# Kernel tuning notes

Hardware: AMD Instinct MI355X
Metric: run time of the kernel (lower is better)

The kernel has to match this reference:

```python
import jax, jax.numpy as jnp
import numpy as np

B, S, D_IN, D_H = 8, 4096, 256, 512
EPS = 1e-6


def setup_inputs() -> dict:
    key = jax.random.key(0)
    ks = jax.random.split(key, 5)
    scale = 1.0 / np.sqrt(D_IN)  # torch Linear default init scale (uniform bound)
    x = jax.random.normal(ks[0], (B, S, D_IN), dtype=jnp.float32)
    Wi = jax.random.normal(ks[1], (D_IN, D_H), dtype=jnp.float32) * scale
    Wf = jax.random.normal(ks[2], (D_IN, D_H), dtype=jnp.float32) * scale
    Wo = jax.random.normal(ks[3], (D_IN, D_H), dtype=jnp.float32) * scale
    Wz = jax.random.normal(ks[4], (D_IN, D_H), dtype=jnp.float32) * scale
    zb = jnp.zeros((D_H,), dtype=jnp.float32)
    return {"x": x, "Wi": Wi, "bi": zb, "Wf": Wf, "bf": zb,
            "Wo": Wo, "bo": zb, "Wz": Wz, "bz": zb}


def _xlstm_forward(x, Wi, bi, Wf, bf, Wo, bo, Wz, bz):
    # Batched projections over all timesteps at once: [B,S,D_H] each.
    i_t = jnp.exp(jnp.clip(jnp.einsum('bsd,dh->bsh', x, Wi) + bi, -20.0, 0.0))
    f_t = jnp.exp(jnp.clip(jnp.einsum('bsd,dh->bsh', x, Wf) + bf, -20.0, 0.0))
    o_t = jax.nn.sigmoid(jnp.einsum('bsd,dh->bsh', x, Wo) + bo)
    z_t = jnp.tanh(jnp.einsum('bsd,dh->bsh', x, Wz) + bz)

    def step(carry, gates):
        c, n = carry
        i, f, o, z = gates
        c = f * c + i * z
        n = f * n + i
        h = o * (c / (n + EPS))
        return (c, n), h

    c0 = jnp.zeros((x.shape[0], Wi.shape[1]), dtype=x.dtype)
    n0 = jnp.ones((x.shape[0], Wi.shape[1]), dtype=x.dtype)
    # time-major scan over the recurrence
    gates_tm = tuple(jnp.swapaxes(g, 0, 1) for g in (i_t, f_t, o_t, z_t))  # [S,B,H]
    _, h_tm = jax.lax.scan(step, (c0, n0), gates_tm)
    return jnp.swapaxes(h_tm, 0, 1)  # [B,S,H]


def reference(x, Wi, bi, Wf, bf, Wo, bo, Wz, bz):
    return _xlstm_forward(x, Wi, bi, Wf, bf, Wo, bo, Wz, bz)
```

## Files before the change

kernel.cpp:

```cpp
#include <hip/hip_runtime.h>
#include <hip/hip_bf16.h>
#include <cstdint>
#include <cstddef>

typedef __hip_bfloat16 bf16;
typedef __attribute__((ext_vector_type(8))) short short8;
typedef __attribute__((ext_vector_type(4))) short short4v;
typedef __attribute__((ext_vector_type(4))) float floatx4;

#define BB 8
#define SS 4096
#define DIN 256
#define DH 512
#define NCH 256
#define CHUNK 16

__device__ __forceinline__ float b2f(bf16 v) { return __bfloat162float(v); }
__device__ __forceinline__ float sh2f(short v) {
    unsigned int u = ((unsigned int)(unsigned short)v) << 16;
    float f; __builtin_memcpy(&f, &u, 4); return f;
}
__device__ __forceinline__ float frcp(float x) { return __builtin_amdgcn_rcpf(x); }

__global__ __launch_bounds__(256) void convert_x(
    const float* __restrict__ X, bf16* __restrict__ Xb)
{
    const int idx = blockIdx.x * 256 + threadIdx.x;
    float4 v = ((const float4*)X)[idx];
    bf16 o[4] = {__float2bfloat16(v.x), __float2bfloat16(v.y),
                 __float2bfloat16(v.z), __float2bfloat16(v.w)};
    ((short4v*)Xb)[idx] = *(const short4v*)o;
}

__global__ __launch_bounds__(256) void transpose_w(
    const float* __restrict__ Wi, const float* __restrict__ Wf,
    const float* __restrict__ Wo, const float* __restrict__ Wz,
    bf16* __restrict__ Wt)
{
    int o  = blockIdx.x * 256 + threadIdx.x;
    int nf = o >> 8;
    int k  = o & 255;
    int g  = nf >> 9;
    int hh = nf & 511;
    const float* W = (g == 0) ? Wi : (g == 1) ? Wf : (g == 2) ? Wo : Wz;
    Wt[o] = __float2bfloat16(W[(size_t)k * DH + hh]);
}

__device__ __forceinline__ void load16_lds(const bf16* g, short* l)
{
    __builtin_amdgcn_global_load_lds(
        (const __attribute__((address_space(1))) unsigned int*)g,
        (__attribute__((address_space(3))) unsigned int*)l,
        16, 0, 0);
}

__global__ __launch_bounds__(256) void gemm_fused(
    const bf16* __restrict__ Xb, const bf16* __restrict__ Wt,
    const float* __restrict__ bi, const float* __restrict__ bfv,
    const float* __restrict__ bo, const float* __restrict__ bz,
    bf16* __restrict__ Pi, bf16* __restrict__ Pf,
    bf16* __restrict__ Po, bf16* __restrict__ Pz,
    float* __restrict__ Aa, float* __restrict__ Bca, float* __restrict__ Bna,
    int nb)
{
    __shared__ __align__(16) short As[64 * 32];
    __shared__ __align__(16) short Bs[256 * 32];
    __shared__ __align__(16) bf16  Gb[4 * 64 * 64];

    const int tid  = threadIdx.x;
    const int m0   = blockIdx.x * 64;
    const int h0   = blockIdx.y * 64;
    const int wave = tid >> 6, lane = tid & 63;
    const int l15  = lane & 15;
    const int q    = lane >> 4;

    floatx4 acc[4][4];
#pragma unroll
    for (int i = 0; i < 4; i++)
#pragma unroll
        for (int j = 0; j < 4; j++) acc[i][j] = (floatx4){0.f, 0.f, 0.f, 0.f};

    const int rr = tid >> 2;
    const int cc = (tid & 3) * 8;
    const bf16* agp = Xb + (size_t)(m0 + rr) * DIN + cc;
    const bf16* bgp0 = Wt + (size_t)(0 * 512 + h0 + rr) * DIN + cc;
    const bf16* bgp1 = Wt + (size_t)(1 * 512 + h0 + rr) * DIN + cc;
    const bf16* bgp2 = Wt + (size_t)(2 * 512 + h0 + rr) * DIN + cc;
    const bf16* bgp3 = Wt + (size_t)(3 * 512 + h0 + rr) * DIN + cc;

    for (int k0 = 0; k0 < DIN; k0 += 32) {
        load16_lds(agp + k0, &As[tid * 8]);
        load16_lds(bgp0 + k0, &Bs[0 * 2048 + tid * 8]);
        load16_lds(bgp1 + k0, &Bs[1 * 2048 + tid * 8]);
        load16_lds(bgp2 + k0, &Bs[2 * 2048 + tid * 8]);
        load16_lds(bgp3 + k0, &Bs[3 * 2048 + tid * 8]);
        __syncthreads();

        short8 af[4], bfr[4];
#pragma unroll
        for (int ti = 0; ti < 4; ti++)
            af[ti] = *(const short8*)&As[(ti * 16 + l15) * 32 + q * 8];
#pragma unroll
        for (int tj = 0; tj < 4; tj++)
            bfr[tj] = *(const short8*)&Bs[wave * 2048 + (tj * 16 + l15) * 32 + q * 8];
#pragma unroll
        for (int ti = 0; ti < 4; ti++)
#pragma unroll
            for (int tj = 0; tj < 4; tj++)
                acc[ti][tj] = __builtin_amdgcn_mfma_f32_16x16x32_bf16(
                    af[ti], bfr[tj], acc[ti][tj], 0, 0, 0);
        __syncthreads();
    }

    const float* bias = (wave == 0) ? bi : (wave == 1) ? bfv
                      : (wave == 2) ? bo : bz;
    bf16* gb = &Gb[wave * 4096];
#pragma unroll
    for (int ti = 0; ti < 4; ti++) {
#pragma unroll
        for (int tj = 0; tj < 4; tj++) {
            const int h = tj * 16 + l15;
            const float bsv = bias[h0 + h];
#pragma unroll
            for (int r = 0; r < 4; r++) {
                const int s = ti * 16 + q * 4 + r;
                const float v = acc[ti][tj][r] + bsv;
                float a;
                if (wave == 0 || wave == 1)
                    a = __expf(fminf(fmaxf(v, -20.f), 0.f));
                else if (wave == 2)
                    a = frcp(1.f + __expf(-v));
                else
                    a = 1.f - 2.f * frcp(__expf(2.f * v) + 1.f);
                gb[s * 64 + h] = __float2bfloat16(a);
            }
        }
    }
    __syncthreads();

    bf16* const planes[4] = {Pi, Pf, Po, Pz};
#pragma unroll
    for (int p = 0; p < 8; p++) {
        const int cid = p * 256 + tid;
        const int g   = cid >> 9;
        const int rem = cid & 511;
        const int s   = rem >> 3;
        const int c   = rem & 7;
        short8 v8 = *(const short8*)&Gb[g * 4096 + s * 64 + c * 8];
        *(short8*)&planes[g][(size_t)(m0 + s) * DH + h0 + c * 8] = v8;
    }

    {
        const int hh  = tid & 63;
        const int sub = tid >> 6;
        float A = 1.f, Bc = 0.f, Bn = 0.f;
#pragma unroll
        for (int s = 0; s < CHUNK; s++) {
            const int sl = sub * CHUNK + s;
            const float f  = b2f(Gb[1 * 4096 + sl * 64 + hh]);
            const float iv = b2f(Gb[0 * 4096 + sl * 64 + hh]);
            const float zv = b2f(Gb[3 * 4096 + sl * 64 + hh]);
            Bc = fmaf(f, Bc, iv * zv);
            Bn = fmaf(f, Bn, iv);
            A *= f;
        }
        const int b  = m0 >> 12;
        const int s0 = m0 & (SS - 1);
        const int ch = (s0 >> 4) + sub;
        const size_t cidx = ((size_t)ch * nb + b) * DH + h0 + hh;
        Aa[cidx] = A; Bca[cidx] = Bc; Bna[cidx] = Bn;
    }
}

__global__ __launch_bounds__(256) void scan_chunks(
    const float* __restrict__ Aa, const float* __restrict__ Bca,
    const float* __restrict__ Bna,
    float* __restrict__ Cs, float* __restrict__ Ns, int nb)
{
    const int t = blockIdx.x * 256 + threadIdx.x;
    float c = 0.f, n = 1.f;
    for (int ch = 0; ch < NCH; ch++) {
        const size_t cidx = (size_t)ch * (nb * DH) + t;
        Cs[cidx] = c; Ns[cidx] = n;
        const float A = Aa[cidx];
        c = fmaf(A, c, Bca[cidx]);
        n = fmaf(A, n, Bna[cidx]);
    }
}

__global__ __launch_bounds__(256) void scan_emit(
    const bf16* __restrict__ Pi, const bf16* __restrict__ Pf,
    const bf16* __restrict__ Po, const bf16* __restrict__ Pz,
    const float* __restrict__ Cs, const float* __restrict__ Ns,
    float* __restrict__ out, int nb)
{
    const int tid = threadIdx.x;
    const int ch  = blockIdx.x * 4 + (tid >> 6);
    const int b   = blockIdx.y;
    const int hg  = (tid & 63) * 8;
    const size_t base = ((size_t)(b * SS + ch * CHUNK)) * DH + hg;
    const size_t cidx = (size_t)(ch * nb + b) * DH + hg;

    float c[8], n[8];
#pragma unroll
    for (int j = 0; j < 2; j++) {
        *(floatx4*)&c[j * 4] = *(const floatx4*)(Cs + cidx + j * 4);
        *(floatx4*)&n[j * 4] = *(const floatx4*)(Ns + cidx + j * 4);
    }

#pragma unroll 4
    for (int s = 0; s < CHUNK; s++) {
        const size_t o = base + (size_t)s * DH;
        short8 i8 = *(const short8*)(Pi + o);
        short8 f8 = *(const short8*)(Pf + o);
        short8 o8 = *(const short8*)(Po + o);
        short8 z8 = *(const short8*)(Pz + o);
        float h[8];
#pragma unroll
        for (int j = 0; j < 8; j++) {
            const float f  = sh2f(f8[j]);
            const float iv = sh2f(i8[j]);
            const float ov = sh2f(o8[j]);
            const float zv = sh2f(z8[j]);
            c[j] = fmaf(f, c[j], iv * zv);
            n[j] = fmaf(f, n[j], iv);
            h[j] = ov * c[j] * frcp(n[j] + 1e-6f);
        }
        *(floatx4*)(out + o)     = *(floatx4*)&h[0];
        *(floatx4*)(out + o + 4) = *(floatx4*)&h[4];
    }
}

extern "C" void kernel_launch(void* const* d_in, const int* in_sizes, int n_in,
                              void* d_out, int out_size, void* d_ws, size_t ws_size,
                              hipStream_t stream)
{
    const float* x   = (const float*)d_in[0];
    const float* Wi  = (const float*)d_in[1];
    const float* bi  = (const float*)d_in[2];
    const float* Wf  = (const float*)d_in[3];
    const float* bfv = (const float*)d_in[4];
    const float* Wo  = (const float*)d_in[5];
    const float* bo  = (const float*)d_in[6];
    const float* Wz  = (const float*)d_in[7];
    const float* bz  = (const float*)d_in[8];
    float* out = (float*)d_out;

    int nb = BB;
    while (nb > 1) {
        size_t need = (1u << 20)
                    + (size_t)nb * SS * DIN * 2
                    + 4 * (size_t)nb * SS * DH * 2
                    + 5 * (size_t)NCH * nb * DH * 4;
        if (need <= ws_size) break;
        nb >>= 1;
    }

    const size_t plane = (size_t)nb * SS * DH;
    bf16* Wt = (bf16*)d_ws;
    bf16* Xb = (bf16*)((char*)d_ws + (1u << 20));
    bf16* Pi = Xb + (size_t)nb * SS * DIN;
    bf16* Pf = Pi + plane;
    bf16* Po = Pf + plane;
    bf16* Pz = Po + plane;
    float* Aa  = (float*)(Pz + plane);
    float* Bca = Aa  + (size_t)NCH * nb * DH;
    float* Bna = Bca + (size_t)NCH * nb * DH;
    float* Cs  = Bna + (size_t)NCH * nb * DH;
    float* Ns  = Cs  + (size_t)NCH * nb * DH;

    transpose_w<<<2048, 256, 0, stream>>>(Wi, Wf, Wo, Wz, Wt);

    for (int b0 = 0; b0 < BB; b0 += nb) {
        const float* Xsrc = x   + (size_t)b0 * SS * DIN;
        float*       Ob   = out + (size_t)b0 * SS * DH;
        convert_x<<<nb * 1024, 256, 0, stream>>>(Xsrc, Xb);
        gemm_fused<<<dim3(nb * SS / 64, DH / 64), 256, 0, stream>>>(
            Xb, Wt, bi, bfv, bo, bz, Pi, Pf, Po, Pz, Aa, Bca, Bna, nb);
        scan_chunks<<<2 * nb, 256, 0, stream>>>(Aa, Bca, Bna, Cs, Ns, nb);
        scan_emit<<<dim3(NCH / 4, nb), 256, 0, stream>>>(
            Pi, Pf, Po, Pz, Cs, Ns, Ob, nb);
    }
}
```

Before: 253.3 us.

## Recompute gate GEMM in emit pass instead of storing bf16 gate planes

The gate projections are no longer written to four bf16 planes in global memory. A first GEMM pass computes only the i, f and z gates to build per-chunk carries, and a second pass recomputes all four gates and emits the output directly using the scanned chunk states. The weight transpose now uses a shared-memory tiled transpose and is merged with the x conversion into a single prep launch. This trades about 1.75x the GEMM FLOPs for removing roughly 32 MB of plane writes and 32 MB of plane reads.

```diff
diff --git a/kernel.cpp b/kernel.cpp
--- a/kernel.cpp
+++ b/kernel.cpp
@@ -16,34 +16,49 @@
 #define CHUNK 16
 
 __device__ __forceinline__ float b2f(bf16 v) { return __bfloat162float(v); }
-__device__ __forceinline__ float sh2f(short v) {
-    unsigned int u = ((unsigned int)(unsigned short)v) << 16;
-    float f; __builtin_memcpy(&f, &u, 4); return f;
-}
 __device__ __forceinline__ float frcp(float x) { return __builtin_amdgcn_rcpf(x); }
 
-__global__ __launch_bounds__(256) void convert_x(
-    const float* __restrict__ X, bf16* __restrict__ Xb)
-{
-    const int idx = blockIdx.x * 256 + threadIdx.x;
-    float4 v = ((const float4*)X)[idx];
-    bf16 o[4] = {__float2bfloat16(v.x), __float2bfloat16(v.y),
-                 __float2bfloat16(v.z), __float2bfloat16(v.w)};
-    ((short4v*)Xb)[idx] = *(const short4v*)o;
-}
-
-__global__ __launch_bounds__(256) void transpose_w(
+__global__ __launch_bounds__(256) void prep(
+    const float* __restrict__ X, bf16* __restrict__ Xb,
     const float* __restrict__ Wi, const float* __restrict__ Wf,
     const float* __restrict__ Wo, const float* __restrict__ Wz,
-    bf16* __restrict__ Wt)
-{
-    int o  = blockIdx.x * 256 + threadIdx.x;
-    int nf = o >> 8;
-    int k  = o & 255;
-    int g  = nf >> 9;
-    int hh = nf & 511;
+    bf16* __restrict__ Wt, int nconv)
+{
+    __shared__ float tile[32][33];
+    const int tid = threadIdx.x;
+    if ((int)blockIdx.x < nconv) {
+        const int idx = blockIdx.x * 256 + tid;
+        float4 v = ((const float4*)X)[idx];
+        bf16 o[4] = {__float2bfloat16(v.x), __float2bfloat16(v.y),
+                     __float2bfloat16(v.z), __float2bfloat16(v.w)};
+        ((short4v*)Xb)[idx] = *(const short4v*)o;
+        return;
+    }
+    const int beta = blockIdx.x - nconv;
+    const int g   = beta >> 7;
+    const int rem = beta & 127;
+    const int k0  = (rem >> 4) * 32;
+    const int h0  = (rem & 15) * 32;
     const float* W = (g == 0) ? Wi : (g == 1) ? Wf : (g == 2) ? Wo : Wz;
-    Wt[o] = __float2bfloat16(W[(size_t)k * DH + hh]);
+
+    {
+        const int r = tid >> 5;
+        const int c = tid & 31;
+#pragma unroll
+        for (int j = 0; j < 4; j++)
+            tile[r + j * 8][c] = W[(size_t)(k0 + r + j * 8) * DH + h0 + c];
+    }
+    __syncthreads();
+    {
+        const int kw = tid & 31;
+        const int hw = tid >> 5;
+#pragma unroll
+        for (int j = 0; j < 4; j++) {
+            const int h = hw + j * 8;
+            Wt[(size_t)(g * 512 + h0 + h) * DIN + k0 + kw] =
+                __float2bfloat16(tile[kw][h]);
+        }
+    }
 }
 
 __device__ __forceinline__ void load16_lds(const bf16* g, short* l)
@@ -54,18 +69,16 @@
         16, 0, 0);
 }
 
-__global__ __launch_bounds__(256) void gemm_fused(
+__global__ __launch_bounds__(256) void gemm_carry(
     const bf16* __restrict__ Xb, const bf16* __restrict__ Wt,
     const float* __restrict__ bi, const float* __restrict__ bfv,
-    const float* __restrict__ bo, const float* __restrict__ bz,
-    bf16* __restrict__ Pi, bf16* __restrict__ Pf,
-    bf16* __restrict__ Po, bf16* __restrict__ Pz,
+    const float* __restrict__ bz,
     float* __restrict__ Aa, float* __restrict__ Bca, float* __restrict__ Bna,
     int nb)
 {
     __shared__ __align__(16) short As[64 * 32];
-    __shared__ __align__(16) short Bs[256 * 32];
-    __shared__ __align__(16) bf16  Gb[4 * 64 * 64];
+    __shared__ __align__(16) short Bs[3 * 64 * 32];
+    __shared__ __align__(16) bf16  Gb[3 * 64 * 64];
 
     const int tid  = threadIdx.x;
     const int m0   = blockIdx.x * 64;
@@ -73,6 +86,7 @@
     const int wave = tid >> 6, lane = tid & 63;
     const int l15  = lane & 15;
     const int q    = lane >> 4;
+    const int gslice = (wave == 3) ? 2 : wave;
 
     floatx4 acc[4][4];
 #pragma unroll
@@ -82,14 +96,133 @@
 
     const int rr = tid >> 2;
     const int cc = (tid & 3) * 8;
-    const bf16* agp = Xb + (size_t)(m0 + rr) * DIN + cc;
+    const bf16* agp  = Xb + (size_t)(m0 + rr) * DIN + cc;
+    const bf16* bgpi = Wt + (size_t)(0 * 512 + h0 + rr) * DIN + cc;
+    const bf16* bgpf = Wt + (size_t)(1 * 512 + h0 + rr) * DIN + cc;
+    const bf16* bgpz = Wt + (size_t)(3 * 512 + h0 + rr) * DIN + cc;
+
+    for (int k0 = 0; k0 < DIN; k0 += 32) {
+        load16_lds(agp  + k0, &As[tid * 8]);
+        load16_lds(bgpi + k0, &Bs[0 * 2048 + tid * 8]);
+        load16_lds(bgpf + k0, &Bs[1 * 2048 + tid * 8]);
+        load16_lds(bgpz + k0, &Bs[2 * 2048 + tid * 8]);
+        __syncthreads();
+
+        if (wave != 2) {
+            short8 af[4], bfr[4];
+#pragma unroll
+            for (int ti = 0; ti < 4; ti++)
+                af[ti] = *(const short8*)&As[(ti * 16 + l15) * 32 + q * 8];
+#pragma unroll
+            for (int tj = 0; tj < 4; tj++)
+                bfr[tj] = *(const short8*)&Bs[gslice * 2048 + (tj * 16 + l15) * 32 + q * 8];
+#pragma unroll
+            for (int ti = 0; ti < 4; ti++)
+#pragma unroll
+                for (int tj = 0; tj < 4; tj++)
+                    acc[ti][tj] = __builtin_amdgcn_mfma_f32_16x16x32_bf16(
+                        af[ti], bfr[tj], acc[ti][tj], 0, 0, 0);
+        }
+        __syncthreads();
+    }
+
+    if (wave != 2) {
+        const float* bias = (wave == 0) ? bi : (wave == 1) ? bfv : bz;
+        bf16* gb = &Gb[gslice * 4096];
+#pragma unroll
+        for (int ti = 0; ti < 4; ti++) {
+#pragma unroll
+            for (int tj = 0; tj < 4; tj++) {
+                const int h = tj * 16 + l15;
+                const float bsv = bias[h0 + h];
+#pragma unroll
+                for (int r = 0; r < 4; r++) {
+                    const int s = ti * 16 + q * 4 + r;
+                    const float v = acc[ti][tj][r] + bsv;
+                    float a;
+                    if (wave == 0 || wave == 1)
+                        a = __expf(fminf(fmaxf(v, -20.f), 0.f));
+                    else
+                        a = 1.f - 2.f * frcp(__expf(2.f * v) + 1.f);
+                    gb[s * 64 + h] = __float2bfloat16(a);
+                }
+            }
+        }
+    }
+    __syncthreads();
+
+    {
+        const int hh  = tid & 63;
+        const int sub = tid >> 6;
+        float A = 1.f, Bc = 0.f, Bn = 0.f;
+#pragma unroll
+        for (int s = 0; s < CHUNK; s++) {
+            const int sl = sub * CHUNK + s;
+            const float iv = b2f(Gb[0 * 4096 + sl * 64 + hh]);
+            const float f  = b2f(Gb[1 * 4096 + sl * 64 + hh]);
+            const float zv = b2f(Gb[2 * 4096 + sl * 64 + hh]);
+            Bc = fmaf(f, Bc, iv * zv);
+            Bn = fmaf(f, Bn, iv);
+            A *= f;
+        }
+        const int b  = m0 >> 12;
+        const int s0 = m0 & (SS - 1);
+        const int ch = (s0 >> 4) + sub;
+        const size_t cidx = ((size_t)ch * nb + b) * DH + h0 + hh;
+        Aa[cidx] = A; Bca[cidx] = Bc; Bna[cidx] = Bn;
+    }
+}
+
+__global__ __launch_bounds__(256) void scan_chunks(
+    const float* __restrict__ Aa, const float* __restrict__ Bca,
+    const float* __restrict__ Bna,
+    float* __restrict__ Cs, float* __restrict__ Ns, int nb)
+{
+    const int t = blockIdx.x * 256 + threadIdx.x;
+    float c = 0.f, n = 1.f;
+    for (int ch = 0; ch < NCH; ch++) {
+        const size_t cidx = (size_t)ch * (nb * DH) + t;
+        Cs[cidx] = c; Ns[cidx] = n;
+        const float A = Aa[cidx];
+        c = fmaf(A, c, Bca[cidx]);
+        n = fmaf(A, n, Bna[cidx]);
+    }
+}
+
+__global__ __launch_bounds__(256) void gemm_emit(
+    const bf16* __restrict__ Xb, const bf16* __restrict__ Wt,
+    const float* __restrict__ bi, const float* __restrict__ bfv,
+    const float* __restrict__ bo, const float* __restrict__ bz,
+    const float* __restrict__ Cs, const float* __restrict__ Ns,
+    float* __restrict__ out, int nb)
+{
+    __shared__ __align__(16) short As[64 * 32];
+    __shared__ __align__(16) short Bs[4 * 64 * 32];
+    __shared__ __align__(16) bf16  Gb[4 * 64 * 64];
+
+    const int tid  = threadIdx.x;
+    const int m0   = blockIdx.x * 64;
+    const int h0   = blockIdx.y * 64;
+    const int wave = tid >> 6, lane = tid & 63;
+    const int l15  = lane & 15;
+    const int q    = lane >> 4;
+
+    floatx4 acc[4][4];
+#pragma unroll
+    for (int i = 0; i < 4; i++)
+#pragma unroll
+        for (int j = 0; j < 4; j++) acc[i][j] = (floatx4){0.f, 0.f, 0.f, 0.f};
+
+    const int rr = tid >> 2;
+    const int cc = (tid & 3) * 8;
+    const bf16* agp  = Xb + (size_t)(m0 + rr) * DIN + cc;
     const bf16* bgp0 = Wt + (size_t)(0 * 512 + h0 + rr) * DIN + cc;
     const bf16* bgp1 = Wt + (size_t)(1 * 512 + h0 + rr) * DIN + cc;
     const bf16* bgp2 = Wt + (size_t)(2 * 512 + h0 + rr) * DIN + cc;
     const bf16* bgp3 = Wt + (size_t)(3 * 512 + h0 + rr) * DIN + cc;
 
     for (int k0 = 0; k0 < DIN; k0 += 32) {
-        load16_lds(agp + k0, &As[tid * 8]);
+        load16_lds(agp  + k0, &As[tid * 8]);
         load16_lds(bgp0 + k0, &Bs[0 * 2048 + tid * 8]);
         load16_lds(bgp1 + k0, &Bs[1 * 2048 + tid * 8]);
         load16_lds(bgp2 + k0, &Bs[2 * 2048 + tid * 8]);
@@ -138,96 +271,25 @@
     }
     __syncthreads();
 
-    bf16* const planes[4] = {Pi, Pf, Po, Pz};
-#pragma unroll
-    for (int p = 0; p < 8; p++) {
-        const int cid = p * 256 + tid;
-        const int g   = cid >> 9;
-        const int rem = cid & 511;
-        const int s   = rem >> 3;
-        const int c   = rem & 7;
-        short8 v8 = *(const short8*)&Gb[g * 4096 + s * 64 + c * 8];
-        *(short8*)&planes[g][(size_t)(m0 + s) * DH + h0 + c * 8] = v8;
-    }
-
     {
         const int hh  = tid & 63;
         const int sub = tid >> 6;
-        float A = 1.f, Bc = 0.f, Bn = 0.f;
+        const int b   = m0 >> 12;
+        const int s0  = m0 & (SS - 1);
+        const int ch  = (s0 >> 4) + sub;
+        const size_t cidx = ((size_t)ch * nb + b) * DH + h0 + hh;
+        float c = Cs[cidx], n = Ns[cidx];
 #pragma unroll
         for (int s = 0; s < CHUNK; s++) {
             const int sl = sub * CHUNK + s;
+            const float iv = b2f(Gb[0 * 4096 + sl * 64 + hh]);
             const float f  = b2f(Gb[1 * 4096 + sl * 64 + hh]);
-            const float iv = b2f(Gb[0 * 4096 + sl * 64 + hh]);
+            const float ov = b2f(Gb[2 * 4096 + sl * 64 + hh]);
             const float zv = b2f(Gb[3 * 4096 + sl * 64 + hh]);
-            Bc = fmaf(f, Bc, iv * zv);
-            Bn = fmaf(f, Bn, iv);
-            A *= f;
-        }
-        const int b  = m0 >> 12;
-        const int s0 = m0 & (SS - 1);
-        const int ch = (s0 >> 4) + sub;
-        const size_t cidx = ((size_t)ch * nb + b) * DH + h0 + hh;
-        Aa[cidx] = A; Bca[cidx] = Bc; Bna[cidx] = Bn;
-    }
-}
-
-__global__ __launch_bounds__(256) void scan_chunks(
-    const float* __restrict__ Aa, const float* __restrict__ Bca,
-    const float* __restrict__ Bna,
-    float* __restrict__ Cs, float* __restrict__ Ns, int nb)
-{
-    const int t = blockIdx.x * 256 + threadIdx.x;
-    float c = 0.f, n = 1.f;
-    for (int ch = 0; ch < NCH; ch++) {
-        const size_t cidx = (size_t)ch * (nb * DH) + t;
-        Cs[cidx] = c; Ns[cidx] = n;
-        const float A = Aa[cidx];
-        c = fmaf(A, c, Bca[cidx]);
-        n = fmaf(A, n, Bna[cidx]);
-    }
-}
-
-__global__ __launch_bounds__(256) void scan_emit(
-    const bf16* __restrict__ Pi, const bf16* __restrict__ Pf,
-    const bf16* __restrict__ Po, const bf16* __restrict__ Pz,
-    const float* __restrict__ Cs, const float* __restrict__ Ns,
-    float* __restrict__ out, int nb)
-{
-    const int tid = threadIdx.x;
-    const int ch  = blockIdx.x * 4 + (tid >> 6);
-    const int b   = blockIdx.y;
-    const int hg  = (tid & 63) * 8;
-    const size_t base = ((size_t)(b * SS + ch * CHUNK)) * DH + hg;
-    const size_t cidx = (size_t)(ch * nb + b) * DH + hg;
-
-    float c[8], n[8];
-#pragma unroll
-    for (int j = 0; j < 2; j++) {
-        *(floatx4*)&c[j * 4] = *(const floatx4*)(Cs + cidx + j * 4);
-        *(floatx4*)&n[j * 4] = *(const floatx4*)(Ns + cidx + j * 4);
-    }
-
-#pragma unroll 4
-    for (int s = 0; s < CHUNK; s++) {
-        const size_t o = base + (size_t)s * DH;
-        short8 i8 = *(const short8*)(Pi + o);
-        short8 f8 = *(const short8*)(Pf + o);
-        short8 o8 = *(const short8*)(Po + o);
-        short8 z8 = *(const short8*)(Pz + o);
-        float h[8];
-#pragma unroll
-        for (int j = 0; j < 8; j++) {
-            const float f  = sh2f(f8[j]);
-            const float iv = sh2f(i8[j]);
-            const float ov = sh2f(o8[j]);
-            const float zv = sh2f(z8[j]);
-            c[j] = fmaf(f, c[j], iv * zv);
-            n[j] = fmaf(f, n[j], iv);
-            h[j] = ov * c[j] * frcp(n[j] + 1e-6f);
-        }
-        *(floatx4*)(out + o)     = *(floatx4*)&h[0];
-        *(floatx4*)(out + o + 4) = *(floatx4*)&h[4];
+            c = fmaf(f, c, iv * zv);
+            n = fmaf(f, n, iv);
+            out[(size_t)(m0 + sl) * DH + h0 + hh] = ov * c * frcp(n + 1e-6f);
+        }
     }
 }
 
@@ -250,35 +312,30 @@
     while (nb > 1) {
         size_t need = (1u << 20)
                     + (size_t)nb * SS * DIN * 2
-                    + 4 * (size_t)nb * SS * DH * 2
                     + 5 * (size_t)NCH * nb * DH * 4;
         if (need <= ws_size) break;
         nb >>= 1;
     }
 
-    const size_t plane = (size_t)nb * SS * DH;
     bf16* Wt = (bf16*)d_ws;
     bf16* Xb = (bf16*)((char*)d_ws + (1u << 20));
-    bf16* Pi = Xb + (size_t)nb * SS * DIN;
-    bf16* Pf = Pi + plane;
-    bf16* Po = Pf + plane;
-    bf16* Pz = Po + plane;
-    float* Aa  = (float*)(Pz + plane);
+    float* Aa  = (float*)(Xb + (size_t)nb * SS * DIN);
     float* Bca = Aa  + (size_t)NCH * nb * DH;
     float* Bna = Bca + (size_t)NCH * nb * DH;
     float* Cs  = Bna + (size_t)NCH * nb * DH;
     float* Ns  = Cs  + (size_t)NCH * nb * DH;
 
-    transpose_w<<<2048, 256, 0, stream>>>(Wi, Wf, Wo, Wz, Wt);
-
     for (int b0 = 0; b0 < BB; b0 += nb) {
         const float* Xsrc = x   + (size_t)b0 * SS * DIN;
         float*       Ob   = out + (size_t)b0 * SS * DH;
-        convert_x<<<nb * 1024, 256, 0, stream>>>(Xsrc, Xb);
-        gemm_fused<<<dim3(nb * SS / 64, DH / 64), 256, 0, stream>>>(
-            Xb, Wt, bi, bfv, bo, bz, Pi, Pf, Po, Pz, Aa, Bca, Bna, nb);
+        const int nconv = nb * 1024;
+        const int ntr   = (b0 == 0) ? 512 : 0;
+        prep<<<nconv + ntr, 256, 0, stream>>>(
+            Xsrc, Xb, Wi, Wf, Wo, Wz, Wt, nconv);
+        gemm_carry<<<dim3(nb * SS / 64, DH / 64), 256, 0, stream>>>(
+            Xb, Wt, bi, bfv, bz, Aa, Bca, Bna, nb);
         scan_chunks<<<2 * nb, 256, 0, stream>>>(Aa, Bca, Bna, Cs, Ns, nb);
-        scan_emit<<<dim3(NCH / 4, nb), 256, 0, stream>>>(
-            Pi, Pf, Po, Pz, Cs, Ns, Ob, nb);
-    }
-}
+        gemm_emit<<<dim3(nb * SS / 64, DH / 64), 256, 0, stream>>>(
+            Xb, Wt, bi, bfv, bo, bz, Cs, Ns, Ob, nb);
+    }
+}
```

New measurement: 263.8 us. 1.04x slower.
